# Kernel optimization log

Measured on AMD Instinct MI355X. Metric: run time of the kernel, lower is better.

The kernel has to match this reference:

```python
import jax, jax.numpy as jnp
import numpy as np

# --- hyperparameters (match init_kwargs / torch defaults) ---
BLOCK_SIZE = 11
MAX_DISP = 48
CONF_TH = 0.3
DS = 2
ALPHA = 0.85          # photometric SSIM weight
GT_TH = 2.0           # GT anchor threshold
SIGN_W, MAG_W = 0.3, 0.7
W_GT, W_PHOTO, W_SIGNMAG, W_SMOOTH = 1.0, 1.0, 0.5, 0.1


def _avg_pool(x, k, stride, pad):
    # torch F.avg_pool2d with count_include_pad=True (default): zero-padded sum / k^2
    s = jax.lax.reduce_window(x, 0.0, jax.lax.add, (1, 1, k, k), (1, 1, stride, stride),
                              ((0, 0), (0, 0), (pad, pad), (pad, pad)))
    return s / (k * k)


def _ssim(x, y):
    C1, C2 = 0.01 ** 2, 0.03 ** 2
    p = lambda t: _avg_pool(t, 3, 1, 1)
    mx, my = p(x), p(y)
    sx = jnp.maximum(p(x * x) - mx * mx, 0.0)
    sy = jnp.maximum(p(y * y) - my * my, 0.0)
    sxy = p(x * y) - mx * my
    n = (2 * mx * my + C1) * (2 * sxy + C2)
    d = (mx * mx + my * my + C1) * (sx + sy + C2)
    return jnp.clip((1 - n / d) / 2, 0.0, 1.0)


def _gt_anchor(pred, gt, conf, occ):
    pos = (gt > GT_TH).astype(pred.dtype)
    trust = conf * occ * pos
    return (trust * jnp.abs(pred - gt)).sum() / jnp.maximum(trust.sum(), 1.0)


def _photometric(disp, left, right):
    B, C, H, W = left.shape
    xb = jnp.arange(W, dtype=disp.dtype)[None, None, None, :]
    xs = xb - disp                                   # sampling x coord (grid_sample, align_corners=True)
    xc = jnp.clip(xs, 0.0, W - 1.0)                  # padding_mode='border'
    x0 = jnp.floor(xc)
    w = xc - x0
    x0i = x0.astype(jnp.int32)
    x1i = jnp.minimum(x0i + 1, W - 1)
    gather = lambda idx: jnp.take_along_axis(right, jnp.broadcast_to(idx, (B, C, H, W)), axis=3)
    warped = gather(x0i) * (1.0 - w) + gather(x1i) * w   # y grid is identity under align_corners
    valid = ((xs > 0) & (xs < W - 1)).astype(disp.dtype)
    l1 = jnp.abs(left - warped).mean(axis=1, keepdims=True)
    ss = _ssim(left, warped).mean(axis=1, keepdims=True)
    err = ALPHA * ss + (1.0 - ALPHA) * l1
    return (err * valid).sum() / jnp.maximum(valid.sum(), 1.0)


def _compute_ncc_disp(left, right):
    B, C, Ho, Wo = left.shape
    lg = _avg_pool(left, DS, DS, 0).mean(axis=1, keepdims=True)   # half-res grayscale
    rg = _avg_pool(right, DS, DS, 0).mean(axis=1, keepdims=True)
    H, W = lg.shape[2], lg.shape[3]
    md = MAX_DISP // DS
    bs, pad = BLOCK_SIZE, BLOCK_SIZE // 2
    p = lambda t: _avg_pool(t, bs, 1, pad)
    lm = p(lg)
    ls = jnp.sqrt(jnp.maximum(p(lg * lg) - lm * lm, 1e-8))
    best_c = jnp.full((B, 1, H, W), -1.0, dtype=jnp.float32)
    best_d = jnp.zeros((B, 1, H, W), dtype=jnp.float32)
    for d in range(-md, md + 1):          # fixed small set of shift offsets
        if d == 0:
            continue
        if d > 0:
            rs = jnp.pad(rg[:, :, :, d:], ((0, 0), (0, 0), (0, 0), (0, d)))
        else:
            rs = jnp.pad(rg[:, :, :, :W + d], ((0, 0), (0, 0), (0, 0), (-d, 0)))
        rm = p(rs)
        rstd = jnp.sqrt(jnp.maximum(p(rs * rs) - rm * rm, 1e-8))
        cross = p(lg * rs)
        ncc = (cross - lm * rm) / (ls * rstd + 1e-8)
        better = ncc > best_c
        best_c = jnp.where(better, ncc, best_c)
        best_d = jnp.where(better, jnp.float32(d), best_d)
    nd = best_d * float(DS)
    nc = jnp.maximum(best_c, 0.0)
    # nearest upsample back to full res (exact integer factor)
    nd = jnp.repeat(jnp.repeat(nd, DS, axis=2), DS, axis=3)
    nc = jnp.repeat(jnp.repeat(nc, DS, axis=2), DS, axis=3)
    nc = nc * (nc > CONF_TH).astype(nc.dtype)
    return jax.lax.stop_gradient(nd), jax.lax.stop_gradient(nc)   # torch @no_grad


def _sign_magnitude(pred, left, right):
    nd, nc = _compute_ncc_disp(left, right)
    active = (nc > 0).astype(pred.dtype)
    n = jnp.maximum(active.sum(), 1.0)
    sign_map = jnp.sign(nd) * active
    l_sign = (jnp.maximum(-pred * sign_map, 0.0) * active).sum() / n
    l_mag = (nc * jnp.abs(pred - nd) * active).sum() / n
    return SIGN_W * l_sign + MAG_W * l_mag


def _smoothness(disp, img):
    ddx = jnp.abs(disp[:, :, :, 1:] - disp[:, :, :, :-1])
    ddy = jnp.abs(disp[:, :, 1:, :] - disp[:, :, :-1, :])
    idx = jnp.abs(img[:, :, :, 1:] - img[:, :, :, :-1]).mean(axis=1, keepdims=True)
    idy = jnp.abs(img[:, :, 1:, :] - img[:, :, :-1, :]).mean(axis=1, keepdims=True)
    return (ddx * jnp.exp(-idx)).mean() + (ddy * jnp.exp(-idy)).mean()


def _total_loss(pred, gt, conf, occ, left, right):
    return (W_GT * _gt_anchor(pred, gt, conf, occ)
            + W_PHOTO * _photometric(pred, left, right)
            + W_SIGNMAG * _sign_magnitude(pred, left, right)
            + W_SMOOTH * _smoothness(pred, left))


def setup_inputs() -> dict:
    key = jax.random.key(0)
    k = jax.random.split(key, 6)
    B, H, W = 4, 544, 960
    return {
        "pred_disp": jax.random.normal(k[0], (B, 1, H, W), dtype=jnp.float32) * 8.0,
        "gt_disp": jax.random.uniform(k[1], (B, 1, H, W), dtype=jnp.float32) * 20.0,
        "gt_conf": jax.random.uniform(k[2], (B, 1, H, W), dtype=jnp.float32),
        "gt_occ": jax.random.uniform(k[3], (B, 1, H, W), dtype=jnp.float32),
        "left_img": jax.random.uniform(k[4], (B, 3, H, W), dtype=jnp.float32),
        "right_img": jax.random.uniform(k[5], (B, 3, H, W), dtype=jnp.float32),
    }


def reference(pred_disp, gt_disp, gt_conf, gt_occ, left_img, right_img):
    return _total_loss(pred_disp, gt_disp, gt_conf, gt_occ, left_img, right_img)
```

## Files before the change

kernel.cpp:

```cpp
#include <hip/hip_runtime.h>
#include <hip/hip_bf16.h>

constexpr int B  = 4;
constexpr int H  = 544;
constexpr int W  = 960;
constexpr int H2 = 272;
constexpr int W2 = 480;
constexpr int NH = B * H2 * W2;
constexpr int NF = B * H * W;

constexpr int TPW = 64, TPH = 16;
constexpr int SW = TPW + 2, SH = TPH + 2;
constexpr int NSTAGE = SW * SH;
constexpr int GX = W / TPW;
constexpr int GY = H / TPH;
constexpr int NBLK  = GX * GY * B;
constexpr int NBLK3 = 8 * 34 * B;

__device__ inline float waveSum(float v) {
  #pragma unroll
  for (int off = 32; off > 0; off >>= 1) v += __shfl_down(v, off, 64);
  return v;
}

__global__ __launch_bounds__(1024) void k_pix(const float* __restrict__ pred,
                                              const float* __restrict__ gt,
                                              const float* __restrict__ conf,
                                              const float* __restrict__ occ,
                                              const float* __restrict__ left,
                                              const float* __restrict__ right,
                                              float* __restrict__ lg,
                                              float* __restrict__ rg,
                                              double* __restrict__ acc) {
  const int bx = blockIdx.x % GX;
  const int by = (blockIdx.x / GX) % GY;
  const int b  = blockIdx.x / (GX * GY);
  const int x0 = bx * TPW, y0 = by * TPH;
  const int tid = threadIdx.x;

  const float* dispb = pred + (size_t)b * H * W;
  const float* lb = left  + (size_t)b * 3 * H * W;
  const float* rb = right + (size_t)b * 3 * H * W;

  __shared__ float4 L4s[NSTAGE];
  __shared__ float4 W4s[NSTAGE];

  for (int e = tid; e < NSTAGE; e += 1024) {
    int r = e / SW, c = e % SW;
    int yy = y0 - 1 + r, xx = x0 - 1 + c;
    float4 l4 = make_float4(0.f, 0.f, 0.f, 0.f);
    float4 w4 = make_float4(0.f, 0.f, 0.f, 0.f);
    if (yy >= 0 && yy < H && xx >= 0 && xx < W) {
      float dv = dispb[yy * W + xx];
      float xsv = (float)xx - dv;
      float xc = fminf(fmaxf(xsv, 0.f), (float)(W - 1));
      float x0f = floorf(xc);
      float w = xc - x0f;
      int x0i = (int)x0f;
      int x1i = min(x0i + 1, W - 1);
      const float* l0 = lb + (size_t)yy * W;
      const float* r0 = rb + (size_t)yy * W;
      l4.x = l0[xx];
      l4.y = l0[(size_t)H * W + xx];
      l4.z = l0[2 * (size_t)H * W + xx];
      l4.w = dv;
      w4.x = r0[x0i] * (1.f - w) + r0[x1i] * w;
      w4.y = r0[(size_t)H * W + x0i] * (1.f - w) + r0[(size_t)H * W + x1i] * w;
      w4.z = r0[2 * (size_t)H * W + x0i] * (1.f - w) + r0[2 * (size_t)H * W + x1i] * w;
    }
    L4s[e] = l4; W4s[e] = w4;
  }
  __syncthreads();

  if (tid < 256) {
    int hx = tid & 31, hy = tid >> 5;
    int y2g = (y0 >> 1) + hy, x2g = (x0 >> 1) + hx;
    int i00 = (2 * hy + 1) * SW + (2 * hx + 1);
    float4 a00 = L4s[i00], a01 = L4s[i00 + 1], a10 = L4s[i00 + SW], a11 = L4s[i00 + SW + 1];
    float sl = 0.f;
    sl += a00.x + a01.x + a10.x + a11.x;
    sl += a00.y + a01.y + a10.y + a11.y;
    sl += a00.z + a01.z + a10.z + a11.z;
    float sr = 0.f;
    int yy2 = y0 + 2 * hy, xx2 = x0 + 2 * hx;
    #pragma unroll
    for (int c = 0; c < 3; c++) {
      const float* rp = rb + (size_t)(c * H + yy2) * W + xx2;
      sr += rp[0] + rp[1] + rp[W] + rp[W + 1];
    }
    size_t ho = (size_t)b * (H2 * W2) + (size_t)y2g * W2 + x2g;
    lg[ho] = sl * (1.f / 12.f);
    rg[ho] = sr * (1.f / 12.f);
  }

  float v[6];
  #pragma unroll
  for (int s = 0; s < 6; s++) v[s] = 0.f;

  {
    const int tx = tid & 63, ty = tid >> 6;
    const int x = x0 + tx, y = y0 + ty;
    const size_t gidx = (size_t)b * H * W + (size_t)y * W + x;
    const int ci = (ty + 1) * SW + (tx + 1);

    float sl[3] = {0,0,0}, sw[3] = {0,0,0}, sl2[3] = {0,0,0},
          sw2[3] = {0,0,0}, slw[3] = {0,0,0};
    float4 cl4, cw4, rl4, dl4;
    #pragma unroll
    for (int dy = -1; dy <= 1; dy++) {
      #pragma unroll
      for (int dx = -1; dx <= 1; dx++) {
        int ni = ci + dy * SW + dx;
        float4 a = L4s[ni];
        float4 wv = W4s[ni];
        sl[0] += a.x;  sl2[0] += a.x * a.x;  sw[0] += wv.x;  sw2[0] += wv.x * wv.x;  slw[0] += a.x * wv.x;
        sl[1] += a.y;  sl2[1] += a.y * a.y;  sw[1] += wv.y;  sw2[1] += wv.y * wv.y;  slw[1] += a.y * wv.y;
        sl[2] += a.z;  sl2[2] += a.z * a.z;  sw[2] += wv.z;  sw2[2] += wv.z * wv.z;  slw[2] += a.z * wv.z;
        if (dy == 0 && dx == 0) { cl4 = a; cw4 = wv; }
        if (dy == 0 && dx == 1) rl4 = a;
        if (dy == 1 && dx == 0) dl4 = a;
      }
    }
    float ds = cl4.w;

    {
      float g = gt[gidx];
      float trust = (g > 2.0f) ? conf[gidx] * occ[gidx] : 0.f;
      v[0] = trust * fabsf(ds - g);
      v[1] = trust;
    }

    {
      float xs = (float)x - ds;
      bool valid = (xs > 0.f) && (xs < (float)(W - 1));
      float cl[3] = {cl4.x, cl4.y, cl4.z};
      float cw[3] = {cw4.x, cw4.y, cw4.z};
      float ssm = 0.f, l1m = 0.f;
      #pragma unroll
      for (int c = 0; c < 3; c++) {
        float mx = sl[c] * (1.f / 9.f), my = sw[c] * (1.f / 9.f);
        float sx = fmaxf(sl2[c] * (1.f / 9.f) - mx * mx, 0.f);
        float sy = fmaxf(sw2[c] * (1.f / 9.f) - my * my, 0.f);
        float sxy = slw[c] * (1.f / 9.f) - mx * my;
        float n  = (2.f * mx * my + 1e-4f) * (2.f * sxy + 9e-4f);
        float dd = (mx * mx + my * my + 1e-4f) * (sx + sy + 9e-4f);
        float ss = (1.f - n / dd) * 0.5f;
        ss = fminf(fmaxf(ss, 0.f), 1.f);
        ssm += ss;
        l1m += fabsf(cl[c] - cw[c]);
      }
      ssm *= (1.f / 3.f); l1m *= (1.f / 3.f);
      float err = 0.85f * ssm + 0.15f * l1m;
      if (valid) { v[2] = err; v[3] = 1.f; }
    }

    if (x < W - 1) {
      float ddx = fabsf(rl4.w - ds);
      float idx = fabsf(rl4.x - cl4.x) + fabsf(rl4.y - cl4.y) + fabsf(rl4.z - cl4.z);
      v[4] = ddx * __expf(-idx * (1.f / 3.f));
    }
    if (y < H - 1) {
      float ddy = fabsf(dl4.w - ds);
      float idy = fabsf(dl4.x - cl4.x) + fabsf(dl4.y - cl4.y) + fabsf(dl4.z - cl4.z);
      v[5] = ddy * __expf(-idy * (1.f / 3.f));
    }
  }

  __shared__ float sm[16][6];
  int wave = threadIdx.x >> 6, lane = threadIdx.x & 63;
  #pragma unroll
  for (int s = 0; s < 6; s++) {
    float r = waveSum(v[s]);
    if (lane == 0) sm[wave][s] = r;
  }
  __syncthreads();
  if (threadIdx.x < 6) {
    float t = 0.f;
    #pragma unroll
    for (int q = 0; q < 16; q++) t += sm[q][threadIdx.x];
    atomicAdd(&acc[threadIdx.x], (double)t);
  }
}

__global__ __launch_bounds__(256) void k_ncc(const float* __restrict__ lg,
                                             const float* __restrict__ rg,
                                             const float* __restrict__ pred,
                                             double* __restrict__ acc,
                                             unsigned int* __restrict__ counter,
                                             float* __restrict__ out) {
  const int b = blockIdx.z;
  const int x0 = blockIdx.x * 64;
  const int y0 = blockIdx.y * 8;
  const int tid = threadIdx.x;

  __shared__ __align__(16) float SM[6692];
  float* LGs = SM;
  float* RM  = SM;
  float* RS  = SM + 896;
  float* RGs = SM + 1792;
  float* POOL = SM + 3988;
  float* P1 = SM + 6292;
  float* P2 = SM + 6492;

  const float* lgb = lg + (size_t)b * (H2 * W2);
  const float* rgb = rg + (size_t)b * (H2 * W2);

  for (int e = tid; e < 18 * 74; e += 256) {
    int r = e / 74, c = e % 74;
    int gy = y0 - 5 + r, gxx = x0 - 5 + c;
    LGs[e] = (gy >= 0 && gy < H2 && gxx >= 0 && gxx < W2) ? lgb[gy * W2 + gxx] : 0.f;
  }
  const int col0RG = x0 - 29;
  for (int e = tid; e < 18 * 122; e += 256) {
    int r = e / 122, c = e % 122;
    int gy = y0 - 5 + r, gxx = col0RG + c;
    RGs[e] = (gy >= 0 && gy < H2 && gxx >= 0 && gxx < W2) ? rgb[gy * W2 + gxx] : 0.f;
  }
  __syncthreads();

  const int hg = tid & 7, hr = tid >> 3;
  float lgc[18];
  float* LH1 = POOL;
  float* LH2 = POOL + 1152;
  if (hr < 18) {
    #pragma unroll
    for (int k = 0; k < 18; k++) lgc[k] = LGs[hr * 74 + 8 * hg + k];
    float w1[8], w2[8];
    float s1 = 0.f, s2 = 0.f;
    #pragma unroll
    for (int k = 0; k < 11; k++) { s1 += lgc[k]; s2 += lgc[k] * lgc[k]; }
    w1[0] = s1; w2[0] = s2;
    #pragma unroll
    for (int j = 1; j < 8; j++) {
      s1 += lgc[j + 10] - lgc[j - 1];
      s2 += lgc[j + 10] * lgc[j + 10] - lgc[j - 1] * lgc[j - 1];
      w1[j] = s1; w2[j] = s2;
    }
    *(float4*)&LH1[hr * 64 + 8 * hg]     = make_float4(w1[0], w1[1], w1[2], w1[3]);
    *(float4*)&LH1[hr * 64 + 8 * hg + 4] = make_float4(w1[4], w1[5], w1[6], w1[7]);
    *(float4*)&LH2[hr * 64 + 8 * hg]     = make_float4(w2[0], w2[1], w2[2], w2[3]);
    *(float4*)&LH2[hr * 64 + 8 * hg + 4] = make_float4(w2[4], w2[5], w2[6], w2[7]);
  }
  const bool headT = (x0 == 0);
  const bool tailT = (x0 == 448);
  if (headT || tailT) {
    int gcol0 = headT ? 0 : 456;
    for (int e = tid; e < 8 * 24; e += 256) {
      int y = e / 24, i = e % 24;
      int lc = gcol0 + i - col0RG;
      float v1 = 0.f, v2 = 0.f;
      if (lc >= 0 && lc < 122) {
        #pragma unroll
        for (int dy = 0; dy < 11; dy++) {
          float v = RGs[(y + dy) * 122 + lc];
          v1 += v; v2 += v * v;
        }
      }
      P1[y * 25 + i + 1] = v1;
      P2[y * 25 + i + 1] = v2;
    }
  }
  __syncthreads();

  if ((headT || tailT) && tid < 8) {
    int y = tid;
    float s1 = 0.f, s2 = 0.f;
    P1[y * 25] = 0.f; P2[y * 25] = 0.f;
    for (int k = 0; k < 24; k++) {
      s1 += P1[y * 25 + k + 1]; P1[y * 25 + k + 1] = s1;
      s2 += P2[y * 25 + k + 1]; P2[y * 25 + k + 1] = s2;
    }
  }
  const int vx = tid & 63;
  const int vys = (tid >> 6) * 2;
  float lmS[2], lsS[2];
  {
    float s1 = 0.f, s2 = 0.f;
    #pragma unroll
    for (int dy = 0; dy < 11; dy++) { s1 += LH1[(vys + dy) * 64 + vx]; s2 += LH2[(vys + dy) * 64 + vx]; }
    #pragma unroll
    for (int k = 0; k < 2; k++) {
      if (k) {
        s1 += LH1[(vys + k + 10) * 64 + vx] - LH1[(vys + k - 1) * 64 + vx];
        s2 += LH2[(vys + k + 10) * 64 + vx] - LH2[(vys + k - 1) * 64 + vx];
      }
      float m = s1 * (1.f / 121.f);
      float s = sqrtf(fmaxf(s2 * (1.f / 121.f) - m * m, 1e-8f));
      lmS[k] = m * 121.f;
      lsS[k] = s * 121.f;
    }
  }
  __syncthreads();

  float* VR1 = POOL;
  float* VR2 = POOL + 976;
  if (tid < 244) {
    int c = tid % 122;
    int rr0 = (tid / 122) * 4;
    float s1 = 0.f, s2 = 0.f;
    #pragma unroll
    for (int dy = 0; dy < 11; dy++) {
      float v = RGs[(rr0 + dy) * 122 + c];
      s1 += v; s2 += v * v;
    }
    VR1[rr0 * 122 + c] = s1; VR2[rr0 * 122 + c] = s2;
    #pragma unroll
    for (int k = 1; k < 4; k++) {
      float vin  = RGs[(rr0 + k + 10) * 122 + c];
      float vout = RGs[(rr0 + k - 1) * 122 + c];
      s1 += vin - vout;
      s2 += vin * vin - vout * vout;
      VR1[(rr0 + k) * 122 + c] = s1; VR2[(rr0 + k) * 122 + c] = s2;
    }
  }
  __syncthreads();

  {
    int r = tid >> 5, seg = tid & 31;
    int c0 = seg * 4;
    if (c0 < 112) {
      float s1 = 0.f, s2 = 0.f;
      #pragma unroll
      for (int m = 0; m < 11; m++) { s1 += VR1[r * 122 + c0 + m]; s2 += VR2[r * 122 + c0 + m]; }
      #pragma unroll
      for (int j = 0; j < 4; j++) {
        if (j) {
          s1 += VR1[r * 122 + c0 + j + 10] - VR1[r * 122 + c0 + j - 1];
          s2 += VR2[r * 122 + c0 + j + 10] - VR2[r * 122 + c0 + j - 1];
        }
        float rm = s1 * (1.f / 121.f);
        float rstd = sqrtf(fmaxf(s2 * (1.f / 121.f) - rm * rm, 1e-8f));
        RM[r * 112 + c0 + j] = rm;
        RS[r * 112 + c0 + j] = rstd;
      }
    }
  }
  __syncthreads();

  float* CH0 = POOL;
  float* CH1 = POOL + 1152;
  const int gx = x0 + vx;
  float bnum[2], bden[2], bdd[2];
  #pragma unroll
  for (int k = 0; k < 2; k++) { bnum[k] = -1.f; bden[k] = 1.f; bdd[k] = 0.f; }

  for (int it = 0; it < 24; ++it) {
    const int d0 = (it < 12) ? (2 * it - 24) : (2 * it - 23);
    if (hr < 18) {
      const int c0 = 8 * hg + d0 + 24;
      float rgv[19];
      #pragma unroll
      for (int j = 0; j < 19; j++) rgv[j] = RGs[hr * 122 + c0 + j];
      float ca[8], cb[8];
      float sa = 0.f, sb = 0.f;
      #pragma unroll
      for (int k = 0; k < 11; k++) { sa += lgc[k] * rgv[k]; sb += lgc[k] * rgv[k + 1]; }
      ca[0] = sa; cb[0] = sb;
      #pragma unroll
      for (int j = 1; j < 8; j++) {
        sa += lgc[j + 10] * rgv[j + 10] - lgc[j - 1] * rgv[j - 1];
        sb += lgc[j + 10] * rgv[j + 11] - lgc[j - 1] * rgv[j];
        ca[j] = sa; cb[j] = sb;
      }
      *(float4*)&CH0[hr * 64 + 8 * hg]     = make_float4(ca[0], ca[1], ca[2], ca[3]);
      *(float4*)&CH0[hr * 64 + 8 * hg + 4] = make_float4(ca[4], ca[5], ca[6], ca[7]);
      *(float4*)&CH1[hr * 64 + 8 * hg]     = make_float4(cb[0], cb[1], cb[2], cb[3]);
      *(float4*)&CH1[hr * 64 + 8 * hg + 4] = make_float4(cb[4], cb[5], cb[6], cb[7]);
    }
    __syncthreads();
    {
      float a0 = 0.f, a1 = 0.f;
      #pragma unroll
      for (int dy = 0; dy < 11; dy++) { a0 += CH0[(vys + dy) * 64 + vx]; a1 += CH1[(vys + dy) * 64 + vx]; }
      #pragma unroll
      for (int k = 0; k < 2; k++) {
        if (k) {
          a0 += CH0[(vys + k + 10) * 64 + vx] - CH0[(vys + k - 1) * 64 + vx];
          a1 += CH1[(vys + k + 10) * 64 + vx] - CH1[(vys + k - 1) * 64 + vx];
        }
        #pragma unroll
        for (int h = 0; h < 2; h++) {
          int d = d0 + h;
          float cs = h ? a1 : a0;
          int rvi = vx + d + 24;
          float rm   = RM[(vys + k) * 112 + rvi];
          float rstd = RS[(vys + k) * 112 + rvi];
          bool eh = (d > 0) ? (gx < 5) : (gx > 474);
          if (eh) {
            float rs = rm * 121.f;
            float r2 = (rstd * rstd + rm * rm) * 121.f;
            int a, bI;
            if (d > 0) { a = max(gx - 5 + d, 0); bI = d; }
            else       { a = 24 + d; bI = min(gx + 5 + d, 479) - 455; }
            rs -= P1[(vys + k) * 25 + bI] - P1[(vys + k) * 25 + a];
            r2 -= P2[(vys + k) * 25 + bI] - P2[(vys + k) * 25 + a];
            rm = rs * (1.f / 121.f);
            rstd = sqrtf(fmaxf(r2 * (1.f / 121.f) - rm * rm, 1e-8f));
          }
          float num = __builtin_fmaf(-lmS[k], rm, cs);
          float den = __builtin_fmaf(lsS[k], rstd, 1.21e-6f);
          if (num * bden[k] > bnum[k] * den) { bnum[k] = num; bden[k] = den; bdd[k] = (float)d; }
        }
      }
    }
    __syncthreads();
  }

  float v6 = 0.f, v7 = 0.f, v8 = 0.f;
  if (gx < W2) {
    const float* pb = pred + (size_t)b * H * W;
    #pragma unroll
    for (int k = 0; k < 2; k++) {
      float bc = bnum[k] / bden[k];
      if (bc > 0.3f) {
        float nd = bdd[k] * 2.f;
        float sgn = (nd > 0.f) ? 1.f : ((nd < 0.f) ? -1.f : 0.f);
        const float* p0 = pb + (size_t)(2 * (y0 + vys + k)) * W + 2 * gx;
        float p00 = p0[0], p01 = p0[1];
        float p10 = p0[W], p11 = p0[W + 1];
        v6 += fmaxf(-p00 * sgn, 0.f) + fmaxf(-p01 * sgn, 0.f)
            + fmaxf(-p10 * sgn, 0.f) + fmaxf(-p11 * sgn, 0.f);
        v7 += bc * (fabsf(p00 - nd) + fabsf(p01 - nd)
                  + fabsf(p10 - nd) + fabsf(p11 - nd));
        v8 += 4.f;
      }
    }
  }
  float* red = P1;
  int wave = tid >> 6, lane = tid & 63;
  float r;
  r = waveSum(v6); if (lane == 0) red[wave * 3 + 0] = r;
  r = waveSum(v7); if (lane == 0) red[wave * 3 + 1] = r;
  r = waveSum(v8); if (lane == 0) red[wave * 3 + 2] = r;
  __syncthreads();

  if (tid == 0) {
    float t6 = red[0] + red[3] + red[6] + red[9];
    float t7 = red[1] + red[4] + red[7] + red[10];
    float t8 = red[2] + red[5] + red[8] + red[11];
    double o6 = atomicAdd(&acc[6], (double)t6);
    double o7 = atomicAdd(&acc[7], (double)t7);
    double o8 = atomicAdd(&acc[8], (double)t8);
    asm volatile("" :: "v"(o6), "v"(o7), "v"(o8) : "memory");
    unsigned int old = atomicAdd(counter, 1u);
    if (old == (unsigned int)(NBLK3 - 1)) {
      double a[9];
      #pragma unroll
      for (int s = 0; s < 9; s++)
        a[s] = __hip_atomic_load(&acc[s], __ATOMIC_RELAXED, __HIP_MEMORY_SCOPE_AGENT);
      double gtl = a[0] / fmax(a[1], 1.0);
      double ph  = a[2] / fmax(a[3], 1.0);
      double n   = fmax(a[8], 1.0);
      double smv = 0.3 * (a[6] / n) + 0.7 * (a[7] / n);
      double smo = a[4] * (1.0 / ((double)B * H * (W - 1)))
                 + a[5] * (1.0 / ((double)B * (H - 1) * W));
      out[0] = (float)(gtl + ph + 0.5 * smv + 0.1 * smo);
    }
  }
}

extern "C" void kernel_launch(void* const* d_in, const int* in_sizes, int n_in,
                              void* d_out, int out_size, void* d_ws, size_t ws_size,
                              hipStream_t stream) {
  const float* pred  = (const float*)d_in[0];
  const float* gt    = (const float*)d_in[1];
  const float* conf  = (const float*)d_in[2];
  const float* occ   = (const float*)d_in[3];
  const float* left  = (const float*)d_in[4];
  const float* right = (const float*)d_in[5];
  float* out = (float*)d_out;

  double* acc = (double*)d_ws;
  unsigned int* counter = (unsigned int*)((char*)d_ws + 96);
  float* lg = (float*)((char*)d_ws + 128);
  float* rg = lg + (size_t)NH;

  hipMemsetAsync(d_ws, 0, 128, stream);

  k_pix<<<NBLK, 1024, 0, stream>>>(pred, gt, conf, occ, left, right,
                                   lg, rg, acc);

  dim3 nccGrid(8, 34, B);
  k_ncc<<<nccGrid, 256, 0, stream>>>(lg, rg, pred, acc, counter, out);
}
```

Baseline: 221.0 us.

## Halve NCC tile height to four rows per block and double grid

The NCC kernel now processes 4 output rows per block instead of 8, with each thread handling one row rather than two, and the grid doubles in y. Shared memory shrinks and the block count rises, which should improve occupancy and parallelism. In exchange, the 10-row halo is reloaded and re-reduced for fewer useful rows, so redundant work per output grows. The pixel kernel also unrolls its staging loop and uses float2 loads for the right-image downsample.

```diff
diff --git a/kernel.cpp b/kernel.cpp
--- a/kernel.cpp
+++ b/kernel.cpp
@@ -15,7 +15,7 @@
 constexpr int GX = W / TPW;
 constexpr int GY = H / TPH;
 constexpr int NBLK  = GX * GY * B;
-constexpr int NBLK3 = 8 * 34 * B;
+constexpr int NBLK3 = 8 * 68 * B;
 
 __device__ inline float waveSum(float v) {
   #pragma unroll
@@ -45,30 +45,34 @@
   __shared__ float4 L4s[NSTAGE];
   __shared__ float4 W4s[NSTAGE];
 
-  for (int e = tid; e < NSTAGE; e += 1024) {
-    int r = e / SW, c = e % SW;
-    int yy = y0 - 1 + r, xx = x0 - 1 + c;
-    float4 l4 = make_float4(0.f, 0.f, 0.f, 0.f);
-    float4 w4 = make_float4(0.f, 0.f, 0.f, 0.f);
-    if (yy >= 0 && yy < H && xx >= 0 && xx < W) {
-      float dv = dispb[yy * W + xx];
-      float xsv = (float)xx - dv;
-      float xc = fminf(fmaxf(xsv, 0.f), (float)(W - 1));
-      float x0f = floorf(xc);
-      float w = xc - x0f;
-      int x0i = (int)x0f;
-      int x1i = min(x0i + 1, W - 1);
-      const float* l0 = lb + (size_t)yy * W;
-      const float* r0 = rb + (size_t)yy * W;
-      l4.x = l0[xx];
-      l4.y = l0[(size_t)H * W + xx];
-      l4.z = l0[2 * (size_t)H * W + xx];
-      l4.w = dv;
-      w4.x = r0[x0i] * (1.f - w) + r0[x1i] * w;
-      w4.y = r0[(size_t)H * W + x0i] * (1.f - w) + r0[(size_t)H * W + x1i] * w;
-      w4.z = r0[2 * (size_t)H * W + x0i] * (1.f - w) + r0[2 * (size_t)H * W + x1i] * w;
-    }
-    L4s[e] = l4; W4s[e] = w4;
+  #pragma unroll
+  for (int itst = 0; itst < 2; ++itst) {
+    int e = tid + itst * 1024;
+    if (e < NSTAGE) {
+      int r = e / SW, c = e % SW;
+      int yy = y0 - 1 + r, xx = x0 - 1 + c;
+      float4 l4 = make_float4(0.f, 0.f, 0.f, 0.f);
+      float4 w4 = make_float4(0.f, 0.f, 0.f, 0.f);
+      if (yy >= 0 && yy < H && xx >= 0 && xx < W) {
+        float dv = dispb[yy * W + xx];
+        float xsv = (float)xx - dv;
+        float xc = fminf(fmaxf(xsv, 0.f), (float)(W - 1));
+        float x0f = floorf(xc);
+        float w = xc - x0f;
+        int x0i = (int)x0f;
+        int x1i = min(x0i + 1, W - 1);
+        const float* l0 = lb + (size_t)yy * W;
+        const float* r0 = rb + (size_t)yy * W;
+        l4.x = l0[xx];
+        l4.y = l0[(size_t)H * W + xx];
+        l4.z = l0[2 * (size_t)H * W + xx];
+        l4.w = dv;
+        w4.x = r0[x0i] * (1.f - w) + r0[x1i] * w;
+        w4.y = r0[(size_t)H * W + x0i] * (1.f - w) + r0[(size_t)H * W + x1i] * w;
+        w4.z = r0[2 * (size_t)H * W + x0i] * (1.f - w) + r0[2 * (size_t)H * W + x1i] * w;
+      }
+      L4s[e] = l4; W4s[e] = w4;
+    }
   }
   __syncthreads();
 
@@ -86,7 +90,9 @@
     #pragma unroll
     for (int c = 0; c < 3; c++) {
       const float* rp = rb + (size_t)(c * H + yy2) * W + xx2;
-      sr += rp[0] + rp[1] + rp[W] + rp[W + 1];
+      float2 q0 = *(const float2*)(rp);
+      float2 q1 = *(const float2*)(rp + W);
+      sr += q0.x + q0.y + q1.x + q1.y;
     }
     size_t ho = (size_t)b * (H2 * W2) + (size_t)y2g * W2 + x2g;
     lg[ho] = sl * (1.f / 12.f);
@@ -190,28 +196,28 @@
                                              float* __restrict__ out) {
   const int b = blockIdx.z;
   const int x0 = blockIdx.x * 64;
-  const int y0 = blockIdx.y * 8;
+  const int y0 = blockIdx.y * 4;
   const int tid = threadIdx.x;
 
-  __shared__ __align__(16) float SM[6692];
+  __shared__ __align__(16) float SM[4736];
   float* LGs = SM;
   float* RM  = SM;
-  float* RS  = SM + 896;
-  float* RGs = SM + 1792;
-  float* POOL = SM + 3988;
-  float* P1 = SM + 6292;
-  float* P2 = SM + 6492;
+  float* RS  = SM + 448;
+  float* RGs = SM + 1036;
+  float* POOL = SM + 2744;
+  float* P1 = SM + 4536;
+  float* P2 = SM + 4636;
 
   const float* lgb = lg + (size_t)b * (H2 * W2);
   const float* rgb = rg + (size_t)b * (H2 * W2);
 
-  for (int e = tid; e < 18 * 74; e += 256) {
+  for (int e = tid; e < 14 * 74; e += 256) {
     int r = e / 74, c = e % 74;
     int gy = y0 - 5 + r, gxx = x0 - 5 + c;
     LGs[e] = (gy >= 0 && gy < H2 && gxx >= 0 && gxx < W2) ? lgb[gy * W2 + gxx] : 0.f;
   }
   const int col0RG = x0 - 29;
-  for (int e = tid; e < 18 * 122; e += 256) {
+  for (int e = tid; e < 14 * 122; e += 256) {
     int r = e / 122, c = e % 122;
     int gy = y0 - 5 + r, gxx = col0RG + c;
     RGs[e] = (gy >= 0 && gy < H2 && gxx >= 0 && gxx < W2) ? rgb[gy * W2 + gxx] : 0.f;
@@ -221,8 +227,8 @@
   const int hg = tid & 7, hr = tid >> 3;
   float lgc[18];
   float* LH1 = POOL;
-  float* LH2 = POOL + 1152;
-  if (hr < 18) {
+  float* LH2 = POOL + 896;
+  if (hr < 14) {
     #pragma unroll
     for (int k = 0; k < 18; k++) lgc[k] = LGs[hr * 74 + 8 * hg + k];
     float w1[8], w2[8];
@@ -245,7 +251,7 @@
   const bool tailT = (x0 == 448);
   if (headT || tailT) {
     int gcol0 = headT ? 0 : 456;
-    for (int e = tid; e < 8 * 24; e += 256) {
+    for (int e = tid; e < 4 * 24; e += 256) {
       int y = e / 24, i = e % 24;
       int lc = gcol0 + i - col0RG;
       float v1 = 0.f, v2 = 0.f;
@@ -262,7 +268,7 @@
   }
   __syncthreads();
 
-  if ((headT || tailT) && tid < 8) {
+  if ((headT || tailT) && tid < 4) {
     int y = tid;
     float s1 = 0.f, s2 = 0.f;
     P1[y * 25] = 0.f; P2[y * 25] = 0.f;
@@ -272,58 +278,50 @@
     }
   }
   const int vx = tid & 63;
-  const int vys = (tid >> 6) * 2;
-  float lmS[2], lsS[2];
+  const int row = tid >> 6;
+  float lmS, lsS;
   {
     float s1 = 0.f, s2 = 0.f;
     #pragma unroll
-    for (int dy = 0; dy < 11; dy++) { s1 += LH1[(vys + dy) * 64 + vx]; s2 += LH2[(vys + dy) * 64 + vx]; }
-    #pragma unroll
-    for (int k = 0; k < 2; k++) {
-      if (k) {
-        s1 += LH1[(vys + k + 10) * 64 + vx] - LH1[(vys + k - 1) * 64 + vx];
-        s2 += LH2[(vys + k + 10) * 64 + vx] - LH2[(vys + k - 1) * 64 + vx];
-      }
-      float m = s1 * (1.f / 121.f);
-      float s = sqrtf(fmaxf(s2 * (1.f / 121.f) - m * m, 1e-8f));
-      lmS[k] = m * 121.f;
-      lsS[k] = s * 121.f;
-    }
+    for (int dy = 0; dy < 11; dy++) { s1 += LH1[(row + dy) * 64 + vx]; s2 += LH2[(row + dy) * 64 + vx]; }
+    float m = s1 * (1.f / 121.f);
+    float s = sqrtf(fmaxf(s2 * (1.f / 121.f) - m * m, 1e-8f));
+    lmS = m * 121.f;
+    lsS = s * 121.f;
   }
   __syncthreads();
 
   float* VR1 = POOL;
-  float* VR2 = POOL + 976;
-  if (tid < 244) {
-    int c = tid % 122;
-    int rr0 = (tid / 122) * 4;
+  float* VR2 = POOL + 488;
+  if (tid < 122) {
+    int c = tid;
     float s1 = 0.f, s2 = 0.f;
     #pragma unroll
     for (int dy = 0; dy < 11; dy++) {
-      float v = RGs[(rr0 + dy) * 122 + c];
+      float v = RGs[dy * 122 + c];
       s1 += v; s2 += v * v;
     }
-    VR1[rr0 * 122 + c] = s1; VR2[rr0 * 122 + c] = s2;
+    VR1[c] = s1; VR2[c] = s2;
     #pragma unroll
     for (int k = 1; k < 4; k++) {
-      float vin  = RGs[(rr0 + k + 10) * 122 + c];
-      float vout = RGs[(rr0 + k - 1) * 122 + c];
+      float vin  = RGs[(k + 10) * 122 + c];
+      float vout = RGs[(k - 1) * 122 + c];
       s1 += vin - vout;
       s2 += vin * vin - vout * vout;
-      VR1[(rr0 + k) * 122 + c] = s1; VR2[(rr0 + k) * 122 + c] = s2;
+      VR1[k * 122 + c] = s1; VR2[k * 122 + c] = s2;
     }
   }
   __syncthreads();
 
   {
-    int r = tid >> 5, seg = tid & 31;
-    int c0 = seg * 4;
+    int r = tid >> 6, seg = tid & 63;
+    int c0 = seg * 2;
     if (c0 < 112) {
       float s1 = 0.f, s2 = 0.f;
       #pragma unroll
       for (int m = 0; m < 11; m++) { s1 += VR1[r * 122 + c0 + m]; s2 += VR2[r * 122 + c0 + m]; }
       #pragma unroll
-      for (int j = 0; j < 4; j++) {
+      for (int j = 0; j < 2; j++) {
         if (j) {
           s1 += VR1[r * 122 + c0 + j + 10] - VR1[r * 122 + c0 + j - 1];
           s2 += VR2[r * 122 + c0 + j + 10] - VR2[r * 122 + c0 + j - 1];
@@ -338,15 +336,13 @@
   __syncthreads();
 
   float* CH0 = POOL;
-  float* CH1 = POOL + 1152;
+  float* CH1 = POOL + 896;
   const int gx = x0 + vx;
-  float bnum[2], bden[2], bdd[2];
-  #pragma unroll
-  for (int k = 0; k < 2; k++) { bnum[k] = -1.f; bden[k] = 1.f; bdd[k] = 0.f; }
+  float bnum = -1.f, bden = 1.f, bdd = 0.f;
 
   for (int it = 0; it < 24; ++it) {
     const int d0 = (it < 12) ? (2 * it - 24) : (2 * it - 23);
-    if (hr < 18) {
+    if (hr < 14) {
       const int c0 = 8 * hg + d0 + 24;
       float rgv[19];
       #pragma unroll
@@ -371,36 +367,29 @@
     {
       float a0 = 0.f, a1 = 0.f;
       #pragma unroll
-      for (int dy = 0; dy < 11; dy++) { a0 += CH0[(vys + dy) * 64 + vx]; a1 += CH1[(vys + dy) * 64 + vx]; }
-      #pragma unroll
-      for (int k = 0; k < 2; k++) {
-        if (k) {
-          a0 += CH0[(vys + k + 10) * 64 + vx] - CH0[(vys + k - 1) * 64 + vx];
-          a1 += CH1[(vys + k + 10) * 64 + vx] - CH1[(vys + k - 1) * 64 + vx];
+      for (int dy = 0; dy < 11; dy++) { a0 += CH0[(row + dy) * 64 + vx]; a1 += CH1[(row + dy) * 64 + vx]; }
+      #pragma unroll
+      for (int h = 0; h < 2; h++) {
+        int d = d0 + h;
+        float cs = h ? a1 : a0;
+        int rvi = vx + d + 24;
+        float rm   = RM[row * 112 + rvi];
+        float rstd = RS[row * 112 + rvi];
+        bool eh = (d > 0) ? (gx < 5) : (gx > 474);
+        if (eh) {
+          float rs = rm * 121.f;
+          float r2 = (rstd * rstd + rm * rm) * 121.f;
+          int a, bI;
+          if (d > 0) { a = max(gx - 5 + d, 0); bI = d; }
+          else       { a = 24 + d; bI = min(gx + 5 + d, 479) - 455; }
+          rs -= P1[row * 25 + bI] - P1[row * 25 + a];
+          r2 -= P2[row * 25 + bI] - P2[row * 25 + a];
+          rm = rs * (1.f / 121.f);
+          rstd = sqrtf(fmaxf(r2 * (1.f / 121.f) - rm * rm, 1e-8f));
         }
-        #pragma unroll
-        for (int h = 0; h < 2; h++) {
-          int d = d0 + h;
-          float cs = h ? a1 : a0;
-          int rvi = vx + d + 24;
-          float rm   = RM[(vys + k) * 112 + rvi];
-          float rstd = RS[(vys + k) * 112 + rvi];
-          bool eh = (d > 0) ? (gx < 5) : (gx > 474);
-          if (eh) {
-            float rs = rm * 121.f;
-            float r2 = (rstd * rstd + rm * rm) * 121.f;
-            int a, bI;
-            if (d > 0) { a = max(gx - 5 + d, 0); bI = d; }
-            else       { a = 24 + d; bI = min(gx + 5 + d, 479) - 455; }
-            rs -= P1[(vys + k) * 25 + bI] - P1[(vys + k) * 25 + a];
-            r2 -= P2[(vys + k) * 25 + bI] - P2[(vys + k) * 25 + a];
-            rm = rs * (1.f / 121.f);
-            rstd = sqrtf(fmaxf(r2 * (1.f / 121.f) - rm * rm, 1e-8f));
-          }
-          float num = __builtin_fmaf(-lmS[k], rm, cs);
-          float den = __builtin_fmaf(lsS[k], rstd, 1.21e-6f);
-          if (num * bden[k] > bnum[k] * den) { bnum[k] = num; bden[k] = den; bdd[k] = (float)d; }
-        }
+        float num = __builtin_fmaf(-lmS, rm, cs);
+        float den = __builtin_fmaf(lsS, rstd, 1.21e-6f);
+        if (num * bden > bnum * den) { bnum = num; bden = den; bdd = (float)d; }
       }
     }
     __syncthreads();
@@ -409,21 +398,18 @@
   float v6 = 0.f, v7 = 0.f, v8 = 0.f;
   if (gx < W2) {
     const float* pb = pred + (size_t)b * H * W;
-    #pragma unroll
-    for (int k = 0; k < 2; k++) {
-      float bc = bnum[k] / bden[k];
-      if (bc > 0.3f) {
-        float nd = bdd[k] * 2.f;
-        float sgn = (nd > 0.f) ? 1.f : ((nd < 0.f) ? -1.f : 0.f);
-        const float* p0 = pb + (size_t)(2 * (y0 + vys + k)) * W + 2 * gx;
-        float p00 = p0[0], p01 = p0[1];
-        float p10 = p0[W], p11 = p0[W + 1];
-        v6 += fmaxf(-p00 * sgn, 0.f) + fmaxf(-p01 * sgn, 0.f)
-            + fmaxf(-p10 * sgn, 0.f) + fmaxf(-p11 * sgn, 0.f);
-        v7 += bc * (fabsf(p00 - nd) + fabsf(p01 - nd)
-                  + fabsf(p10 - nd) + fabsf(p11 - nd));
-        v8 += 4.f;
-      }
+    float bc = bnum / bden;
+    if (bc > 0.3f) {
+      float nd = bdd * 2.f;
+      float sgn = (nd > 0.f) ? 1.f : ((nd < 0.f) ? -1.f : 0.f);
+      const float* p0 = pb + (size_t)(2 * (y0 + row)) * W + 2 * gx;
+      float p00 = p0[0], p01 = p0[1];
+      float p10 = p0[W], p11 = p0[W + 1];
+      v6 += fmaxf(-p00 * sgn, 0.f) + fmaxf(-p01 * sgn, 0.f)
+          + fmaxf(-p10 * sgn, 0.f) + fmaxf(-p11 * sgn, 0.f);
+      v7 += bc * (fabsf(p00 - nd) + fabsf(p01 - nd)
+                + fabsf(p10 - nd) + fabsf(p11 - nd));
+      v8 += 4.f;
     }
   }
   float* red = P1;
@@ -480,6 +466,6 @@
   k_pix<<<NBLK, 1024, 0, stream>>>(pred, gt, conf, occ, left, right,
                                    lg, rg, acc);
 
-  dim3 nccGrid(8, 34, B);
+  dim3 nccGrid(8, 68, B);
   k_ncc<<<nccGrid, 256, 0, stream>>>(lg, rg, pred, acc, counter, out);
 }
```

Result: slower. 261.2 us (+18.2%).
